# Performance work log

Measured on AMD Instinct MI355X. Metric: run time of the kernel, lower is better.

## Reference

```python
import jax, jax.numpy as jnp
import numpy as np

N = 50000
E = 400000
F_IN = 128
HID = 64
HEADS = 4
OUT_HEADS = 4
N_CLS = 121
NEG_SLOPE = 0.2


def _gat_layer(x, src, dst, W, a_src, a_dst, b, heads, out_ch, concat):
    n = x.shape[0]
    xh = (x @ W).reshape(n, heads, out_ch)                      # [N,H,C]
    alpha_s = jnp.sum(xh * a_src, axis=-1)                      # [N,H]
    alpha_d = jnp.sum(xh * a_dst, axis=-1)                      # [N,H]
    logits = jax.nn.leaky_relu(alpha_s[src] + alpha_d[dst], NEG_SLOPE)  # [E,H]
    # numerically stable edge softmax per destination node
    m = jax.ops.segment_max(logits, dst, num_segments=n)        # [N,H]
    e = jnp.exp(logits - m[dst])                                # [E,H]
    denom = jax.ops.segment_sum(e, dst, num_segments=n)         # [N,H]
    alpha = e / (denom[dst] + 1e-16)                            # [E,H]
    msg = alpha[:, :, None] * xh[src]                           # [E,H,C]
    out = jax.ops.segment_sum(msg, dst, num_segments=n)         # [N,H,C]
    if concat:
        out = out.reshape(n, heads * out_ch)
    else:
        out = out.mean(axis=1)
    return out + b


def setup_inputs() -> dict:
    key = jax.random.key(0)
    ks = jax.random.split(key, 20)
    x = jax.random.normal(ks[0], (N, F_IN), dtype=jnp.float32)
    edge_index = jax.random.randint(ks[1], (2, E), 0, N, dtype=jnp.int32)
    s = lambda *sh: 1.0 / np.sqrt(sh[0])
    inp = {
        'x': x,
        'edge_index': edge_index,
        # conv1: F_IN -> HEADS*HID
        'W1': jax.random.normal(ks[2], (F_IN, HEADS * HID), jnp.float32) * s(F_IN),
        'a1_src': jax.random.normal(ks[3], (HEADS, HID), jnp.float32) * s(HID),
        'a1_dst': jax.random.normal(ks[4], (HEADS, HID), jnp.float32) * s(HID),
        'b1': jnp.zeros((HEADS * HID,), jnp.float32),
        'lin1_W': jax.random.normal(ks[5], (F_IN, HEADS * HID), jnp.float32) * s(F_IN),
        'lin1_b': jnp.zeros((HEADS * HID,), jnp.float32),
        # conv2: HEADS*HID -> HEADS*HID
        'W2': jax.random.normal(ks[6], (HEADS * HID, HEADS * HID), jnp.float32) * s(HEADS * HID),
        'a2_src': jax.random.normal(ks[7], (HEADS, HID), jnp.float32) * s(HID),
        'a2_dst': jax.random.normal(ks[8], (HEADS, HID), jnp.float32) * s(HID),
        'b2': jnp.zeros((HEADS * HID,), jnp.float32),
        # conv3: HEADS*HID -> N_CLS (mean over OUT_HEADS)
        'W3': jax.random.normal(ks[9], (HEADS * HID, OUT_HEADS * N_CLS), jnp.float32) * s(HEADS * HID),
        'a3_src': jax.random.normal(ks[10], (OUT_HEADS, N_CLS), jnp.float32) * s(N_CLS),
        'a3_dst': jax.random.normal(ks[11], (OUT_HEADS, N_CLS), jnp.float32) * s(N_CLS),
        'b3': jnp.zeros((N_CLS,), jnp.float32),
        'lin3_W': jax.random.normal(ks[12], (HEADS * HID, N_CLS), jnp.float32) * s(HEADS * HID),
        'lin3_b': jnp.zeros((N_CLS,), jnp.float32),
    }
    return inp


def reference(x, edge_index, W1, a1_src, a1_dst, b1, lin1_W, lin1_b,
              W2, a2_src, a2_dst, b2, W3, a3_src, a3_dst, b3, lin3_W, lin3_b):
    src, dst = edge_index[0], edge_index[1]
    h = _gat_layer(x, src, dst, W1, a1_src, a1_dst, b1, HEADS, HID, True) + (x @ lin1_W + lin1_b)
    h = jax.nn.elu(h)
    h = _gat_layer(h, src, dst, W2, a2_src, a2_dst, b2, HEADS, HID, True) + h  # residual skip (no lin2)
    h = jax.nn.elu(h)
    out = _gat_layer(h, src, dst, W3, a3_src, a3_dst, b3, OUT_HEADS, N_CLS, False) + (h @ lin3_W + lin3_b)
    return out
```

## Files before the change

### kernel.cpp

```cpp
#include <hip/hip_runtime.h>
#include <cstdint>
#include <cstddef>

#define F_IN 128
#define HC12 256
#define HC3P 512
#define NCLS 121
#define L3STR 128

typedef unsigned short u16;
typedef unsigned int u32;
typedef __attribute__((ext_vector_type(8))) short short8;
typedef __attribute__((ext_vector_type(8))) __fp16 half8;
typedef __attribute__((ext_vector_type(4))) float float4v;

static __device__ __forceinline__ float lrelu(float x) { return x > 0.f ? x : 0.2f * x; }

static __device__ __forceinline__ u16 f2h(float f) {
    union { __fp16 h; u16 u; } v; v.h = (__fp16)f; return v.u;
}
static __device__ __forceinline__ float h2f(u16 u) {
    union { u16 u; __fp16 h; } v; v.u = u; return (float)v.h;
}

static __device__ __forceinline__ void gload16(const u16* g, u16* l) {
    __builtin_amdgcn_global_load_lds((const __attribute__((address_space(1))) void*)g,
                                     (__attribute__((address_space(3))) void*)l,
                                     16, 0, 0);
}

__global__ void hist_kernel(const int* __restrict__ dst, int* __restrict__ deg, int E) {
    int e = blockIdx.x * 256 + threadIdx.x;
    if (e < E) atomicAdd(&deg[dst[e]], 1);
}

__global__ __launch_bounds__(1024) void scan_kernel(const int* __restrict__ deg,
                                                    int* __restrict__ rowp, int N) {
    __shared__ int swave[16];
    __shared__ int s_carry;
    int tid = threadIdx.x;
    int w = tid >> 6, lane = tid & 63;
    if (tid == 0) { rowp[0] = 0; s_carry = 0; }
    __syncthreads();
    for (int base = 0; base < N; base += 4096) {
        int i0 = base + tid * 4;
        int v0 = (i0     < N) ? deg[i0]     : 0;
        int v1 = (i0 + 1 < N) ? deg[i0 + 1] : 0;
        int v2 = (i0 + 2 < N) ? deg[i0 + 2] : 0;
        int v3 = (i0 + 3 < N) ? deg[i0 + 3] : 0;
        int t = v0 + v1 + v2 + v3;
        int sc = t;
#pragma unroll
        for (int off = 1; off < 64; off <<= 1) {
            int u = __shfl_up(sc, off, 64);
            if (lane >= off) sc += u;
        }
        if (lane == 63) swave[w] = sc;
        __syncthreads();
        if (w == 0) {
            int ws = (lane < 16) ? swave[lane] : 0;
#pragma unroll
            for (int off = 1; off < 16; off <<= 1) {
                int u = __shfl_up(ws, off, 64);
                if (lane >= off) ws += u;
            }
            if (lane < 16) swave[lane] = ws;
        }
        __syncthreads();
        int carry = s_carry;
        int tb = carry + ((w > 0) ? swave[w - 1] : 0) + sc - t;
        if (i0     < N) rowp[i0 + 1] = tb + v0;
        if (i0 + 1 < N) rowp[i0 + 2] = tb + v0 + v1;
        if (i0 + 2 < N) rowp[i0 + 3] = tb + v0 + v1 + v2;
        if (i0 + 3 < N) rowp[i0 + 4] = tb + t;
        __syncthreads();
        if (tid == 1023) s_carry = carry + swave[15];
        __syncthreads();
    }
}

__global__ void scatter_kernel(const int* __restrict__ src, const int* __restrict__ dst,
                               const int* __restrict__ rowp, int* __restrict__ cur,
                               int* __restrict__ col, int E) {
    int e = blockIdx.x * 256 + threadIdx.x;
    if (e < E) {
        int d = dst[e];
        int pos = rowp[d] + atomicAdd(&cur[d], 1);
        col[pos] = src[e];
    }
}

__global__ void cvtT_all_kernel(const float* W1, const float* l1W, const float* W2,
                                const float* W3, const float* l3W,
                                const float* a3s, const float* a3d,
                                u16* C1, u16* C2, u16* C3,
                                float* as3p, float* ad3p) {
    int i = blockIdx.x * 256 + threadIdx.x;
    if (i >= 285952) {
        int j = i - 285952;
        if (j < 1024) {
            int t = j >> 9, k = j & 511;
            int h = k >> 7, c = k & 127;
            const float* a = t ? a3d : a3s;
            float v = (c < NCLS) ? a[h * NCLS + c] : 0.f;
            (t ? ad3p : as3p)[k] = v;
        }
        return;
    }
    const float* B; u16* o; int K, N;
    if (i < 32768)       { B = W1;  o = C1;             K = 128; N = 256; }
    else if (i < 65536)  { B = l1W; o = C1 + 256 * 128; K = 128; N = 256; i -= 32768; }
    else if (i < 131072) { B = W2;  o = C2;             K = 256; N = 256; i -= 65536; }
    else if (i < 254976) { B = W3;  o = C3;             K = 256; N = 484; i -= 131072; }
    else                 { B = l3W; o = C3 + 484 * 256; K = 256; N = 121; i -= 254976; }
    int n = i % N, k = i / N;
    o[(size_t)n * K + k] = f2h(B[(size_t)k * N + n]);
}

__global__ __launch_bounds__(256) void xcvt_kernel(const float* __restrict__ x,
                                                   u16* __restrict__ o, int total8) {
    int i = blockIdx.x * 256 + threadIdx.x;
    if (i >= total8) return;
    const float4* p = (const float4*)(x + (size_t)i * 8);
    float4 a = p[0], b = p[1];
    union { u16 u[8]; short8 v; } r;
    r.u[0] = f2h(a.x); r.u[1] = f2h(a.y); r.u[2] = f2h(a.z); r.u[3] = f2h(a.w);
    r.u[4] = f2h(b.x); r.u[5] = f2h(b.y); r.u[6] = f2h(b.z); r.u[7] = f2h(b.w);
    *(short8*)(o + (size_t)i * 8) = r.v;
}

#define BM 128
#define BN 128
#define BK 32

__global__ __launch_bounds__(256, 3) void gemm_f16(const u16* __restrict__ A16,
                                                   const u16* __restrict__ BT,
                                                   int M, int K, int Ntot,
                                                   int nx, int ny,
                                                   int Nb, u16* __restrict__ Cb, int strideB,
                                                   int pad121,
                                                   u16* __restrict__ Cf16,
                                                   const float* __restrict__ biasf, int strideF) {
    __shared__ __align__(16) u16 sA[BM * BK];
    __shared__ __align__(16) u16 sB[BN * BK];
    int tid = threadIdx.x;
    int wave = tid >> 6, lane = tid & 63;
    int wr = wave >> 1, wc = wave & 1;

    int bid = blockIdx.x;
    int G = nx * 8;
    int g = bid / G;
    int rem = ny - g * 8;
    int rb, cb;
    if (rem >= 8) {
        int r = bid - g * G;
        rb = g * 8 + (r & 7);
        cb = r >> 3;
    } else {
        int t = bid - g * G;
        rb = g * 8 + t % rem;
        cb = t / rem;
    }
    int m0 = rb * BM, n0 = cb * BN;

    int fm = lane & 15;
    int q = lane >> 4;

    int srow = lane >> 2;
    int sch = (lane & 3) * 8;
    u16* lA0 = &sA[(wave * 32) * BK];
    u16* lA1 = &sA[(wave * 32 + 16) * BK];
    u16* lB0 = &sB[(wave * 32) * BK];
    u16* lB1 = &sB[(wave * 32 + 16) * BK];
    int ar0 = min(m0 + wave * 32 + srow, M - 1);
    int ar1 = min(m0 + wave * 32 + 16 + srow, M - 1);
    int br0 = min(n0 + wave * 32 + srow, Ntot - 1);
    int br1 = min(n0 + wave * 32 + 16 + srow, Ntot - 1);

    float4v acc[4][4];
#pragma unroll
    for (int i = 0; i < 4; i++)
#pragma unroll
        for (int j = 0; j < 4; j++) acc[i][j] = (float4v){0.f, 0.f, 0.f, 0.f};

    for (int kc = 0; kc < K; kc += BK) {
        gload16(&A16[(size_t)ar0 * K + kc + sch], lA0);
        gload16(&A16[(size_t)ar1 * K + kc + sch], lA1);
        gload16(&BT[(size_t)br0 * K + kc + sch], lB0);
        gload16(&BT[(size_t)br1 * K + kc + sch], lB1);
        __syncthreads();

        half8 ah[4];
#pragma unroll
        for (int mi = 0; mi < 4; mi++)
            ah[mi] = *(const half8*)&sA[(wr * 64 + mi * 16 + fm) * BK + q * 8];
#pragma unroll
        for (int ni = 0; ni < 4; ni++) {
            half8 bh = *(const half8*)&sB[(wc * 64 + ni * 16 + fm) * BK + q * 8];
#pragma unroll
            for (int mi = 0; mi < 4; mi++)
                acc[mi][ni] = __builtin_amdgcn_mfma_f32_16x16x32_f16(ah[mi], bh, acc[mi][ni], 0, 0, 0);
        }
        __syncthreads();
    }

#pragma unroll
    for (int mi = 0; mi < 4; mi++) {
#pragma unroll
        for (int ni = 0; ni < 4; ni++) {
            int colg = n0 + wc * 64 + ni * 16 + fm;
            if (colg >= Ntot) continue;
            int cg = colg;
            if (pad121 && colg < Nb) {
                int hh = (colg * 1084) >> 17;
                cg = colg + 7 * hh;
            }
#pragma unroll
            for (int r = 0; r < 4; r++) {
                int rowg = m0 + wr * 64 + mi * 16 + q * 4 + r;
                if (rowg >= M) continue;
                float v = acc[mi][ni][r];
                if (colg < Nb) {
                    Cb[(size_t)rowg * strideB + cg] = f2h(v);
                } else {
                    int cf = colg - Nb;
                    Cf16[(size_t)rowg * strideF + cf] = f2h(v + biasf[cf]);
                }
            }
        }
    }
}

__global__ __launch_bounds__(256) void alpha_wave_256(const u16* __restrict__ xh,
                                                      const float* __restrict__ a_s,
                                                      const float* __restrict__ a_d,
                                                      float* __restrict__ as_o,
                                                      float* __restrict__ ad_o, int N) {
    int lane = threadIdx.x & 63;
    int n = blockIdx.x * 4 + (threadIdx.x >> 6);
    if (n >= N) return;
    int c = lane * 4;
    uint2 v = *(const uint2*)&xh[(size_t)n * HC12 + c];
    float4 s4 = *(const float4*)&a_s[c];
    float4 d4 = *(const float4*)&a_d[c];
    float x0 = h2f((u16)(v.x & 0xffff)), x1 = h2f((u16)(v.x >> 16));
    float x2 = h2f((u16)(v.y & 0xffff)), x3 = h2f((u16)(v.y >> 16));
    float ss = x0 * s4.x + x1 * s4.y + x2 * s4.z + x3 * s4.w;
    float sd = x0 * d4.x + x1 * d4.y + x2 * d4.z + x3 * d4.w;
#pragma unroll
    for (int o = 1; o < 16; o <<= 1) {
        ss += __shfl_xor(ss, o, 64);
        sd += __shfl_xor(sd, o, 64);
    }
    if ((lane & 15) == 0) {
        as_o[n * 4 + (lane >> 4)] = ss;
        ad_o[n * 4 + (lane >> 4)] = sd;
    }
}

__global__ __launch_bounds__(256) void alpha3_wave(const u16* __restrict__ xh3,
                                                   const float* __restrict__ as3p,
                                                   const float* __restrict__ ad3p,
                                                   float* __restrict__ as_o,
                                                   float* __restrict__ ad_o, int N) {
    int l = threadIdx.x & 63;
    int n = blockIdx.x * 4 + (threadIdx.x >> 6);
    if (n >= N) return;
    int h = l >> 4, li = l & 15;
    int c0 = li * 8;
    uint4 v = *(const uint4*)&xh3[(size_t)n * HC3P + l * 8];
    float4 s0 = *(const float4*)&as3p[l * 8];
    float4 s1 = *(const float4*)&as3p[l * 8 + 4];
    float4 d0 = *(const float4*)&ad3p[l * 8];
    float4 d1 = *(const float4*)&ad3p[l * 8 + 4];
    u32 ww[4] = {v.x, v.y, v.z, v.w};
    float xs[8];
#pragma unroll
    for (int j = 0; j < 8; j++) {
        float xf = h2f((u16)((ww[j >> 1] >> ((j & 1) * 16)) & 0xffff));
        xs[j] = (c0 + j < NCLS) ? xf : 0.f;
    }
    float ss = xs[0] * s0.x + xs[1] * s0.y + xs[2] * s0.z + xs[3] * s0.w
             + xs[4] * s1.x + xs[5] * s1.y + xs[6] * s1.z + xs[7] * s1.w;
    float sd = xs[0] * d0.x + xs[1] * d0.y + xs[2] * d0.z + xs[3] * d0.w
             + xs[4] * d1.x + xs[5] * d1.y + xs[6] * d1.z + xs[7] * d1.w;
#pragma unroll
    for (int o = 1; o < 16; o <<= 1) {
        ss += __shfl_xor(ss, o, 64);
        sd += __shfl_xor(sd, o, 64);
    }
    if (li == 0) {
        as_o[n * 4 + h] = ss;
        ad_o[n * 4 + h] = sd;
    }
}

__global__ __launch_bounds__(256) void stats_alpha_kernel(const int* __restrict__ rowp,
                                                          const int* __restrict__ col,
                                                          const float* __restrict__ asrc,
                                                          const float* __restrict__ adst,
                                                          float* __restrict__ alphaE, int N) {
    int i = blockIdx.x * 256 + threadIdx.x;
    if (i >= N * 4) return;
    int n = i >> 2, h = i & 3;
    int r0 = rowp[n], r1 = rowp[n + 1];
    float ad = adst[i];
    float m = -3.4e38f, s = 0.f;
    for (int e = r0; e < r1; e++) {
        int sc = col[e];
        float l = lrelu(asrc[sc * 4 + h] + ad);
        float nm = fmaxf(m, l);
        s = s * __expf(m - nm) + __expf(l - nm);
        m = nm;
    }
    float rd = 1.f / (s + 1e-16f);
    for (int e = r0; e < r1; e++) {
        int sc = col[e];
        float l = lrelu(asrc[sc * 4 + h] + ad);
        alphaE[(size_t)e * 4 + h] = __expf(l - m) * rd;
    }
}

__global__ __launch_bounds__(256) void agg_wave_256(const u16* __restrict__ xh,
                                                    const int* __restrict__ rowp,
                                                    const int* __restrict__ col,
                                                    const float* __restrict__ alphaE,
                                                    const float* __restrict__ bias,
                                                    const u16* __restrict__ res16,
                                                    u16* __restrict__ out16, int N) {
    int l = threadIdx.x & 63;
    int n = blockIdx.x * 4 + (threadIdx.x >> 6);
    if (n >= N) return;
    int r0 = rowp[n], r1 = rowp[n + 1];
    int s = l >> 5, li = l & 31;
    int c = li * 8;
    int h = li >> 3;
    float acc[8] = {0.f, 0.f, 0.f, 0.f, 0.f, 0.f, 0.f, 0.f};
    for (int kb = r0; kb < r1; kb += 16) {
        int cn = min(16, r1 - kb);
        int cidx = col[kb + (l & 15)];
        float alv = alphaE[(size_t)kb * 4 + l];
        int npair = (cn + 1) >> 1;
#pragma unroll 4
        for (int k = 0; k < npair; k++) {
            int e = 2 * k + s;
            int em = e < cn ? e : cn - 1;
            int src = __shfl(cidx, em, 64);
            float al = __shfl(alv, em * 4 + h, 64);
            if (e >= cn) al = 0.f;
            uint4 v = *(const uint4*)&xh[(size_t)src * HC12 + c];
            acc[0] += al * h2f((u16)(v.x & 0xffff));
            acc[1] += al * h2f((u16)(v.x >> 16));
            acc[2] += al * h2f((u16)(v.y & 0xffff));
            acc[3] += al * h2f((u16)(v.y >> 16));
            acc[4] += al * h2f((u16)(v.z & 0xffff));
            acc[5] += al * h2f((u16)(v.z >> 16));
            acc[6] += al * h2f((u16)(v.w & 0xffff));
            acc[7] += al * h2f((u16)(v.w >> 16));
        }
    }
#pragma unroll
    for (int j = 0; j < 8; j++) acc[j] += __shfl_xor(acc[j], 32, 64);
    if (l < 32) {
        uint4 rv = *(const uint4*)&res16[(size_t)n * HC12 + c];
        u32 rw[4] = {rv.x, rv.y, rv.z, rv.w};
        float4 b0 = *(const float4*)&bias[c];
        float4 b1v = *(const float4*)&bias[c + 4];
        float bb[8] = {b0.x, b0.y, b0.z, b0.w, b1v.x, b1v.y, b1v.z, b1v.w};
        union { u16 u[8]; uint4 v; } p;
#pragma unroll
        for (int j = 0; j < 8; j++) {
            float rf = h2f((u16)((rw[j >> 1] >> ((j & 1) * 16)) & 0xffff));
            float vv = acc[j] + bb[j] + rf;
            float ev = vv > 0.f ? vv : expm1f(vv);
            p.u[j] = f2h(ev);
        }
        *(uint4*)&out16[(size_t)n * HC12 + c] = p.v;
    }
}

__global__ __launch_bounds__(256) void agg_wave_out(const u16* __restrict__ xh3,
                                                    const int* __restrict__ rowp,
                                                    const int* __restrict__ col,
                                                    const float* __restrict__ alphaE,
                                                    const float* __restrict__ b3,
                                                    const u16* __restrict__ lin3h,
                                                    float* __restrict__ out, int N) {
    int l = threadIdx.x & 63;
    int n = blockIdx.x * 4 + (threadIdx.x >> 6);
    if (n >= N) return;
    int r0 = rowp[n], r1 = rowp[n + 1];
    int h = l >> 4;
    float acc[8] = {0.f, 0.f, 0.f, 0.f, 0.f, 0.f, 0.f, 0.f};
    for (int kb = r0; kb < r1; kb += 16) {
        int cn = min(16, r1 - kb);
        int cidx = col[kb + (l & 15)];
        float alv = alphaE[(size_t)kb * 4 + l];
#pragma unroll 4
        for (int k = 0; k < cn; k++) {
            int src = __shfl(cidx, k, 64);
            float al = __shfl(alv, k * 4 + h, 64);
            uint4 v = *(const uint4*)&xh3[(size_t)src * HC3P + l * 8];
            acc[0] += al * h2f((u16)(v.x & 0xffff));
            acc[1] += al * h2f((u16)(v.x >> 16));
            acc[2] += al * h2f((u16)(v.y & 0xffff));
            acc[3] += al * h2f((u16)(v.y >> 16));
            acc[4] += al * h2f((u16)(v.z & 0xffff));
            acc[5] += al * h2f((u16)(v.z >> 16));
            acc[6] += al * h2f((u16)(v.w & 0xffff));
            acc[7] += al * h2f((u16)(v.w >> 16));
        }
    }
#pragma unroll
    for (int j = 0; j < 8; j++) {
        acc[j] += __shfl_xor(acc[j], 16, 64);
        acc[j] += __shfl_xor(acc[j], 32, 64);
    }
    if (l < 16) {
        uint4 lv = *(const uint4*)&lin3h[(size_t)n * L3STR + l * 8];
        u32 lw[4] = {lv.x, lv.y, lv.z, lv.w};
        int c0 = l * 8;
#pragma unroll
        for (int j = 0; j < 8; j++) {
            int cc = c0 + j;
            if (cc < NCLS) {
                float lf = h2f((u16)((lw[j >> 1] >> ((j & 1) * 16)) & 0xffff));
                out[(size_t)n * NCLS + cc] = 0.25f * acc[j] + b3[cc] + lf;
            }
        }
    }
}

extern "C" void kernel_launch(void* const* d_in, const int* in_sizes, int n_in,
                              void* d_out, int out_size, void* d_ws, size_t ws_size,
                              hipStream_t stream) {
    const float* x   = (const float*)d_in[0];
    const int*   ei  = (const int*)d_in[1];
    const float* W1  = (const float*)d_in[2];
    const float* a1s = (const float*)d_in[3];
    const float* a1d = (const float*)d_in[4];
    const float* b1  = (const float*)d_in[5];
    const float* l1W = (const float*)d_in[6];
    const float* l1b = (const float*)d_in[7];
    const float* W2  = (const float*)d_in[8];
    const float* a2s = (const float*)d_in[9];
    const float* a2d = (const float*)d_in[10];
    const float* b2  = (const float*)d_in[11];
    const float* W3  = (const float*)d_in[12];
    const float* a3s = (const float*)d_in[13];
    const float* a3d = (const float*)d_in[14];
    const float* b3  = (const float*)d_in[15];
    const float* l3W = (const float*)d_in[16];
    const float* l3b = (const float*)d_in[17];

    const int N = in_sizes[0] / F_IN;
    const int E = in_sizes[1] / 2;
    const int* srcv = ei;
    const int* dstv = ei + E;

    char* ws = (char*)d_ws;
    size_t off = 0;
    auto alloc = [&](size_t bytes) -> char* {
        char* p = ws + off;
        off += (bytes + 255) & ~(size_t)255;
        return p;
    };
    u16*   xh    = (u16*)alloc((size_t)N * HC3P * 2 + 256);
    u16*   x16   = (u16*)alloc((size_t)N * F_IN * 2);
    u16*   h1f   = (u16*)alloc((size_t)N * HC12 * 2);
    u16*   h2f   = (u16*)alloc((size_t)N * HC12 * 2);
    u16*   lin1h = (u16*)alloc((size_t)N * HC12 * 2);
    u16*   lin3h = (u16*)alloc((size_t)N * L3STR * 2);
    float* as_   = (float*)alloc((size_t)N * 4 * 4);
    float* ad_   = (float*)alloc((size_t)N * 4 * 4);
    int* rowp    = (int*)alloc((size_t)(N + 1) * 4);
    int* degc    = (int*)alloc((size_t)N * 4);
    int* cur     = (int*)alloc((size_t)N * 4);
    int* col     = (int*)alloc((size_t)E * 4 + 256);
    float* alphaE = (float*)alloc((size_t)E * 4 * 4 + 256);
    u16* C1 = (u16*)alloc((size_t)512 * 128 * 2);
    u16* C2 = (u16*)alloc((size_t)256 * 256 * 2);
    u16* C3 = (u16*)alloc((size_t)605 * 256 * 2);
    float* as3p = (float*)alloc(512 * 4);
    float* ad3p = (float*)alloc(512 * 4);
    (void)ws_size; (void)n_in; (void)out_size;

    hipMemsetAsync(degc, 0, (size_t)N * 4, stream);
    hipMemsetAsync(cur, 0, (size_t)N * 4, stream);
    hist_kernel<<<(E + 255) / 256, 256, 0, stream>>>(dstv, degc, E);
    scan_kernel<<<1, 1024, 0, stream>>>(degc, rowp, N);
    scatter_kernel<<<(E + 255) / 256, 256, 0, stream>>>(srcv, dstv, rowp, cur, col, E);

    cvtT_all_kernel<<<(285952 + 1024 + 255) / 256, 256, 0, stream>>>(W1, l1W, W2, W3, l3W,
                                                                     a3s, a3d, C1, C2, C3,
                                                                     as3p, ad3p);
    xcvt_kernel<<<(N * F_IN / 8 + 255) / 256, 256, 0, stream>>>(x, x16, N * F_IN / 8);

    int ny = (N + BM - 1) / BM;
    int sgrid = (N * 4 + 255) / 256;
    int wgrid = (N + 3) / 4;

    gemm_f16<<<4 * ny, 256, 0, stream>>>(x16, C1, N, F_IN, 512, 4, ny,
                                         256, xh, 256, 0, lin1h, l1b, 256);
    alpha_wave_256<<<wgrid, 256, 0, stream>>>(xh, a1s, a1d, as_, ad_, N);
    stats_alpha_kernel<<<sgrid, 256, 0, stream>>>(rowp, col, as_, ad_, alphaE, N);
    agg_wave_256<<<wgrid, 256, 0, stream>>>(xh, rowp, col, alphaE, b1, lin1h, h1f, N);

    gemm_f16<<<2 * ny, 256, 0, stream>>>(h1f, C2, N, HC12, 256, 2, ny,
                                         256, xh, 256, 0, nullptr, nullptr, 0);
    alpha_wave_256<<<wgrid, 256, 0, stream>>>(xh, a2s, a2d, as_, ad_, N);
    stats_alpha_kernel<<<sgrid, 256, 0, stream>>>(rowp, col, as_, ad_, alphaE, N);
    agg_wave_256<<<wgrid, 256, 0, stream>>>(xh, rowp, col, alphaE, b2, h1f, h2f, N);

    gemm_f16<<<5 * ny, 256, 0, stream>>>(h2f, C3, N, HC12, 605, 5, ny,
                                         484, xh, HC3P, 1, lin3h, l3b, L3STR);
    alpha3_wave<<<wgrid, 256, 0, stream>>>(xh, as3p, ad3p, as_, ad_, N);
    stats_alpha_kernel<<<sgrid, 256, 0, stream>>>(rowp, col, as_, ad_, alphaE, N);
    agg_wave_out<<<wgrid, 256, 0, stream>>>(xh, rowp, col, alphaE, b3, lin3h, (float*)d_out, N);
}
```

Before: 507.4 us.

## Parallelize edge softmax across wave lanes and pack two nodes per wave in output aggregation

The per-(node,head) serial edge-softmax kernel is replaced by a wave-per-node kernel in which 16 edges × 4 heads map to lanes. Max and sum come from cross-lane shuffle reductions, with a single-pass fast path for degree ≤16. The final aggregation now processes two nodes per wave, each half-wave loading 16 halves per lane in 8-edge chunks. The aim is to remove the serial dependent gather latency and raise memory-level parallelism, at the cost of idle lanes for low-degree nodes and more registers.

```diff
diff --git a/kernel.cpp b/kernel.cpp
--- a/kernel.cpp
+++ b/kernel.cpp
@@ -295,29 +295,58 @@
     }
 }
 
-__global__ __launch_bounds__(256) void stats_alpha_kernel(const int* __restrict__ rowp,
-                                                          const int* __restrict__ col,
-                                                          const float* __restrict__ asrc,
-                                                          const float* __restrict__ adst,
-                                                          float* __restrict__ alphaE, int N) {
-    int i = blockIdx.x * 256 + threadIdx.x;
-    if (i >= N * 4) return;
-    int n = i >> 2, h = i & 3;
+__global__ __launch_bounds__(256) void stats_wave(const int* __restrict__ rowp,
+                                                  const int* __restrict__ col,
+                                                  const float* __restrict__ asrc,
+                                                  const float* __restrict__ adst,
+                                                  float* __restrict__ alphaE, int N) {
+    int l = threadIdx.x & 63;
+    int n = blockIdx.x * 4 + (threadIdx.x >> 6);
+    if (n >= N) return;
     int r0 = rowp[n], r1 = rowp[n + 1];
-    float ad = adst[i];
-    float m = -3.4e38f, s = 0.f;
-    for (int e = r0; e < r1; e++) {
-        int sc = col[e];
-        float l = lrelu(asrc[sc * 4 + h] + ad);
-        float nm = fmaxf(m, l);
-        s = s * __expf(m - nm) + __expf(l - nm);
-        m = nm;
-    }
-    float rd = 1.f / (s + 1e-16f);
-    for (int e = r0; e < r1; e++) {
-        int sc = col[e];
-        float l = lrelu(asrc[sc * 4 + h] + ad);
-        alphaE[(size_t)e * 4 + h] = __expf(l - m) * rd;
+    if (r0 == r1) return;
+    int h = l & 3, el = l >> 2;
+    float ad = adst[n * 4 + h];
+    if (r1 - r0 <= 16) {
+        int e = r0 + el;
+        bool v = e < r1;
+        int sc = col[v ? e : r0];
+        float lg = lrelu(asrc[sc * 4 + h] + ad);
+        float m = v ? lg : -3.4e38f;
+#pragma unroll
+        for (int o = 4; o < 64; o <<= 1) m = fmaxf(m, __shfl_xor(m, o, 64));
+        float ex = v ? __expf(lg - m) : 0.f;
+        float s = ex;
+#pragma unroll
+        for (int o = 4; o < 64; o <<= 1) s += __shfl_xor(s, o, 64);
+        if (v) alphaE[(size_t)e * 4 + h] = ex / (s + 1e-16f);
+    } else {
+        float m = -3.4e38f, s = 0.f;
+        for (int kb = r0; kb < r1; kb += 16) {
+            int e = kb + el;
+            bool v = e < r1;
+            int sc = col[v ? e : r0];
+            float lg = lrelu(asrc[sc * 4 + h] + ad);
+            float cm = v ? lg : -3.4e38f;
+#pragma unroll
+            for (int o = 4; o < 64; o <<= 1) cm = fmaxf(cm, __shfl_xor(cm, o, 64));
+            float nm = fmaxf(m, cm);
+            float ex = v ? __expf(lg - nm) : 0.f;
+            float cs = ex;
+#pragma unroll
+            for (int o = 4; o < 64; o <<= 1) cs += __shfl_xor(cs, o, 64);
+            s = s * __expf(m - nm) + cs;
+            m = nm;
+        }
+        float rd = 1.f / (s + 1e-16f);
+        for (int kb = r0; kb < r1; kb += 16) {
+            int e = kb + el;
+            if (e < r1) {
+                int sc = col[e];
+                float lg = lrelu(asrc[sc * 4 + h] + ad);
+                alphaE[(size_t)e * 4 + h] = __expf(lg - m) * rd;
+            }
+        }
     }
 }
 
@@ -387,41 +416,49 @@
                                                     const u16* __restrict__ lin3h,
                                                     float* __restrict__ out, int N) {
     int l = threadIdx.x & 63;
-    int n = blockIdx.x * 4 + (threadIdx.x >> 6);
-    if (n >= N) return;
-    int r0 = rowp[n], r1 = rowp[n + 1];
-    int h = l >> 4;
-    float acc[8] = {0.f, 0.f, 0.f, 0.f, 0.f, 0.f, 0.f, 0.f};
-    for (int kb = r0; kb < r1; kb += 16) {
-        int cn = min(16, r1 - kb);
-        int cidx = col[kb + (l & 15)];
-        float alv = alphaE[(size_t)kb * 4 + l];
-#pragma unroll 4
-        for (int k = 0; k < cn; k++) {
-            int src = __shfl(cidx, k, 64);
-            float al = __shfl(alv, k * 4 + h, 64);
-            uint4 v = *(const uint4*)&xh3[(size_t)src * HC3P + l * 8];
-            acc[0] += al * h2f((u16)(v.x & 0xffff));
-            acc[1] += al * h2f((u16)(v.x >> 16));
-            acc[2] += al * h2f((u16)(v.y & 0xffff));
-            acc[3] += al * h2f((u16)(v.y >> 16));
-            acc[4] += al * h2f((u16)(v.z & 0xffff));
-            acc[5] += al * h2f((u16)(v.z >> 16));
-            acc[6] += al * h2f((u16)(v.w & 0xffff));
-            acc[7] += al * h2f((u16)(v.w >> 16));
-        }
-    }
-#pragma unroll
-    for (int j = 0; j < 8; j++) {
+    int half = l >> 5, li = l & 31;
+    int bl = l & 32;
+    int n = blockIdx.x * 8 + (threadIdx.x >> 6) * 2 + half;
+    bool nv = n < N;
+    int r0 = nv ? rowp[n] : 0;
+    int r1 = nv ? rowp[n + 1] : 0;
+    float acc[16];
+#pragma unroll
+    for (int j = 0; j < 16; j++) acc[j] = 0.f;
+    for (int kb = r0; kb < r1; kb += 8) {
+        int ec = min(8, r1 - kb);
+        int ce = kb + (li & 7);
+        int cidx = col[ce < r1 ? ce : r0];
+        float alv = alphaE[(size_t)kb * 4 + li];
+        for (int k = 0; k < ec; k++) {
+            int src = __shfl(cidx, bl + k, 64);
+            float al = __shfl(alv, bl + k * 4 + (li >> 3), 64);
+            const u16* row = xh3 + (size_t)src * HC3P + li * 16;
+            uint4 v0 = *(const uint4*)&row[0];
+            uint4 v1 = *(const uint4*)&row[8];
+            u32 w0[4] = {v0.x, v0.y, v0.z, v0.w};
+            u32 w1[4] = {v1.x, v1.y, v1.z, v1.w};
+#pragma unroll
+            for (int jj = 0; jj < 4; jj++) {
+                acc[2 * jj]     += al * h2f((u16)(w0[jj] & 0xffff));
+                acc[2 * jj + 1] += al * h2f((u16)(w0[jj] >> 16));
+                acc[8 + 2 * jj]     += al * h2f((u16)(w1[jj] & 0xffff));
+                acc[8 + 2 * jj + 1] += al * h2f((u16)(w1[jj] >> 16));
+            }
+        }
+    }
+#pragma unroll
+    for (int j = 0; j < 16; j++) {
+        acc[j] += __shfl_xor(acc[j], 8, 64);
         acc[j] += __shfl_xor(acc[j], 16, 64);
-        acc[j] += __shfl_xor(acc[j], 32, 64);
-    }
-    if (l < 16) {
-        uint4 lv = *(const uint4*)&lin3h[(size_t)n * L3STR + l * 8];
-        u32 lw[4] = {lv.x, lv.y, lv.z, lv.w};
-        int c0 = l * 8;
-#pragma unroll
-        for (int j = 0; j < 8; j++) {
+    }
+    if (nv && li < 8) {
+        int c0 = li * 16;
+        uint4 l0 = *(const uint4*)&lin3h[(size_t)n * L3STR + c0];
+        uint4 l1 = *(const uint4*)&lin3h[(size_t)n * L3STR + c0 + 8];
+        u32 lw[8] = {l0.x, l0.y, l0.z, l0.w, l1.x, l1.y, l1.z, l1.w};
+#pragma unroll
+        for (int j = 0; j < 16; j++) {
             int cc = c0 + j;
             if (cc < NCLS) {
                 float lf = h2f((u16)((lw[j >> 1] >> ((j & 1) * 16)) & 0xffff));
@@ -497,24 +534,24 @@
     xcvt_kernel<<<(N * F_IN / 8 + 255) / 256, 256, 0, stream>>>(x, x16, N * F_IN / 8);
 
     int ny = (N + BM - 1) / BM;
-    int sgrid = (N * 4 + 255) / 256;
     int wgrid = (N + 3) / 4;
+    int wgrid8 = (N + 7) / 8;
 
     gemm_f16<<<4 * ny, 256, 0, stream>>>(x16, C1, N, F_IN, 512, 4, ny,
                                          256, xh, 256, 0, lin1h, l1b, 256);
     alpha_wave_256<<<wgrid, 256, 0, stream>>>(xh, a1s, a1d, as_, ad_, N);
-    stats_alpha_kernel<<<sgrid, 256, 0, stream>>>(rowp, col, as_, ad_, alphaE, N);
+    stats_wave<<<wgrid, 256, 0, stream>>>(rowp, col, as_, ad_, alphaE, N);
     agg_wave_256<<<wgrid, 256, 0, stream>>>(xh, rowp, col, alphaE, b1, lin1h, h1f, N);
 
     gemm_f16<<<2 * ny, 256, 0, stream>>>(h1f, C2, N, HC12, 256, 2, ny,
                                          256, xh, 256, 0, nullptr, nullptr, 0);
     alpha_wave_256<<<wgrid, 256, 0, stream>>>(xh, a2s, a2d, as_, ad_, N);
-    stats_alpha_kernel<<<sgrid, 256, 0, stream>>>(rowp, col, as_, ad_, alphaE, N);
+    stats_wave<<<wgrid, 256, 0, stream>>>(rowp, col, as_, ad_, alphaE, N);
     agg_wave_256<<<wgrid, 256, 0, stream>>>(xh, rowp, col, alphaE, b2, h1f, h2f, N);
 
     gemm_f16<<<5 * ny, 256, 0, stream>>>(h2f, C3, N, HC12, 605, 5, ny,
                                          484, xh, HC3P, 1, lin3h, l3b, L3STR);
     alpha3_wave<<<wgrid, 256, 0, stream>>>(xh, as3p, ad3p, as_, ad_, N);
-    stats_alpha_kernel<<<sgrid, 256, 0, stream>>>(rowp, col, as_, ad_, alphaE, N);
-    agg_wave_out<<<wgrid, 256, 0, stream>>>(xh, rowp, col, alphaE, b3, lin3h, (float*)d_out, N);
-}
+    stats_wave<<<wgrid, 256, 0, stream>>>(rowp, col, as_, ad_, alphaE, N);
+    agg_wave_out<<<wgrid8, 256, 0, stream>>>(xh, rowp, col, alphaE, b3, lin3h, (float*)d_out, N);
+}
```

Result: no change. 500.0 us (-1.5%).
